# Optimization experiments

Hardware: AMD Instinct MI355X
Metric: run time of the kernel (lower is better)

Reference implementation:

```python
import math
import jax, jax.numpy as jnp
import numpy as np

B_, H_, L_, N_ = 64, 256, 1024, 64  # batch, n_feat, n_embd(=seq len), complex state modes (d_state=128 -> 64 conj pairs)


def setup_inputs() -> dict:
    key = jax.random.key(0)
    ks = jax.random.split(key, 12)
    x = jax.random.normal(ks[0], (B_, H_, L_), jnp.float32)
    t = jax.random.randint(ks[1], (B_,), 0, 1000)
    # AdaLayerNorm linear: n_embd -> 2*n_embd
    ada_w = jax.random.normal(ks[2], (2 * L_, L_), jnp.float32) * 0.02
    ada_b = jnp.zeros((2 * L_,), jnp.float32)
    # S4Layer prenorm (LayerNorm over n_feat, affine)
    norm_w = jnp.ones((H_,), jnp.float32)
    norm_b = jnp.zeros((H_,), jnp.float32)
    # S4D-style diagonal SSM parameters
    log_dt = math.log(0.001) + jax.random.uniform(ks[3], (H_,), jnp.float32) * (math.log(0.1) - math.log(0.001))
    A_re = jnp.full((H_, N_), math.log(0.5), jnp.float32)            # A_real = -exp(A_re) = -0.5
    A_im = jnp.ones((H_, 1), jnp.float32) * (math.pi * jnp.arange(N_, dtype=jnp.float32))[None, :]
    C_re = jax.random.normal(ks[4], (2, H_, N_), jnp.float32) * (N_ ** -0.5)  # 2 channels: bidirectional
    C_im = jax.random.normal(ks[5], (2, H_, N_), jnp.float32) * (N_ ** -0.5)
    D = jax.random.normal(ks[6], (H_,), jnp.float32)
    out_w = jax.random.normal(ks[7], (H_, H_), jnp.float32) * (H_ ** -0.5)   # S4 output 1x1 conv
    out_b = jnp.zeros((H_,), jnp.float32)
    lin1_w = jax.random.normal(ks[8], (H_, H_), jnp.float32) * (H_ ** -0.5)
    lin1_b = jnp.zeros((H_,), jnp.float32)
    lin2_w = jax.random.normal(ks[9], (H_, H_), jnp.float32) * (H_ ** -0.5)
    lin2_b = jnp.zeros((H_,), jnp.float32)
    return dict(x=x, t=t, ada_w=ada_w, ada_b=ada_b, norm_w=norm_w, norm_b=norm_b,
                log_dt=log_dt, A_re=A_re, A_im=A_im, C_re=C_re, C_im=C_im, D=D,
                out_w=out_w, out_b=out_b, lin1_w=lin1_w, lin1_b=lin1_b,
                lin2_w=lin2_w, lin2_b=lin2_b)


def _ln(v):
    m = v.mean(-1, keepdims=True)
    s = v.var(-1, keepdims=True)
    return (v - m) * jax.lax.rsqrt(s + 1e-5)


def _forward(t, x, ada_w, ada_b, norm_w, norm_b, log_dt, A_re, A_im, C_re, C_im, D,
             out_w, out_b, lin1_w, lin1_b, lin2_w, lin2_b):
    B, H, L = x.shape
    # ---- AdaLayerNorm over last dim (n_embd = L) ----
    half = L // 2
    freqs = jnp.exp(jnp.arange(half, dtype=jnp.float32) * (-math.log(10000.0) / (half - 1)))
    emb = t.astype(jnp.float32)[:, None] * freqs[None, :]
    emb = jnp.concatenate([jnp.sin(emb), jnp.cos(emb)], axis=-1)           # (B, L)
    emb = jax.nn.silu(emb) @ ada_w.T + ada_b                                # (B, 2L)
    scale, shift = jnp.split(emb[:, None, :], 2, axis=2)                    # (B,1,L)
    x = _ln(x) * (1.0 + scale) + shift                                      # (B,H,L)
    # ---- S4Layer: prenorm over channels ----
    z = (_ln(x.transpose(0, 2, 1)) * norm_w + norm_b).transpose(0, 2, 1)    # (B,H,L)
    # ---- S4 (diagonal SSM) bidirectional FFT convolution ----
    dt = jnp.exp(log_dt)                                                    # (H,)
    A = -jnp.exp(A_re) + 1j * A_im                                          # (H,N)
    dtA = dt[:, None] * A
    dA = jnp.exp(dtA)
    C = (C_re + 1j * C_im) * ((dA - 1.0) / A)                               # ZOH-discretized (2,H,N)
    vand = jnp.exp(dtA[:, :, None] * jnp.arange(L, dtype=jnp.float32))      # (H,N,L)
    K = 2.0 * jnp.real(jnp.einsum('chn,hnl->chl', C, vand))                 # (2,H,L)
    k = jnp.pad(K[0], ((0, 0), (0, L))) + jnp.pad(K[1][:, ::-1], ((0, 0), (L, 0)))  # (H,2L)
    n = 2 * L
    y = jnp.fft.irfft(jnp.fft.rfft(z, n=n) * jnp.fft.rfft(k, n=n), n=n)[..., :L]
    y = y + D[:, None] * z
    y = jax.nn.gelu(y, approximate=False)
    y = jnp.einsum('oi,bil->bol', out_w, y) + out_b[None, :, None]          # S4 output 1x1 conv
    x2 = y + x                                                              # residual
    # ---- gated output ----
    g = jnp.tanh(x2) * jax.nn.sigmoid(x2)
    out1 = jnp.einsum('oi,bil->bol', lin1_w, g) + lin1_b[None, :, None] + x
    out2 = jnp.einsum('oi,bil->bol', lin2_w, g) + lin2_b[None, :, None]
    return (out1, out2)


def reference(x, t, ada_w, ada_b, norm_w, norm_b, log_dt, A_re, A_im, C_re, C_im, D,
              out_w, out_b, lin1_w, lin1_b, lin2_w, lin2_b):
    return _forward(t, x, ada_w, ada_b, norm_w, norm_b, log_dt, A_re, A_im, C_re, C_im,
                    D, out_w, out_b, lin1_w, lin1_b, lin2_w, lin2_b)
```

## Files before the change

kernel.cpp:

```cpp
#include <hip/hip_runtime.h>
#include <math.h>

#define Bq 64
#define Hq 256
#define Lq 1024
#define HLq (Hq*Lq)
#define BHLq (Bq*Hq*Lq)
#define HNq (Hq*64)

typedef __attribute__((ext_vector_type(8))) short bf16x8;
typedef __attribute__((ext_vector_type(4))) float f32x4;

__device__ __forceinline__ float sigmoidf_(float x){ return 1.f/(1.f+expf(-x)); }
__device__ __forceinline__ unsigned short f2bf(float f){
  unsigned u = __float_as_uint(f);
  u += 0x7FFF + ((u>>16)&1);
  return (unsigned short)(u>>16);
}
__device__ __forceinline__ float bf2f(unsigned short h){ return __uint_as_float(((unsigned)h)<<16); }

__global__ __launch_bounds__(256) void k_ada2(const int* __restrict__ tptr,
        const float* __restrict__ ada_w, float* __restrict__ Part){
  __shared__ float Es[64][68];
  __shared__ float Ws[64][68];
  const int tid = threadIdx.x;
  const int o0 = blockIdx.x * 64;
  const int kc = blockIdx.y;
  const int k0 = kc * 64;
  const float ci = -logf(10000.f) / 511.f;
  #pragma unroll
  for (int it = 0; it < 4; ++it){
    int fidx = it*256 + tid;
    int row = fidx >> 4;
    int c4  = fidx & 15;
    float tb = (float)tptr[row];
    float4 v;
    float* vp = &v.x;
    #pragma unroll
    for (int q = 0; q < 4; ++q){
      int k = k0 + c4*4 + q;
      float f = expf(ci * (float)(k & 511));
      float arg = tb * f;
      float s = (k < 512) ? sinf(arg) : cosf(arg);
      vp[q] = s * sigmoidf_(s);
    }
    *(float4*)&Es[row][c4*4] = v;
  }
  #pragma unroll
  for (int it = 0; it < 4; ++it){
    int fidx = it*256 + tid;
    int row = fidx >> 4;
    int c4  = fidx & 15;
    *(float4*)&Ws[row][c4*4] = *(const float4*)(ada_w + (size_t)(o0+row)*1024 + k0 + c4*4);
  }
  __syncthreads();
  float acc[4][4] = {};
  #pragma unroll
  for (int ks = 0; ks < 16; ++ks){
    int k = ks*4;
    float4 ev[4], wv[4];
    #pragma unroll
    for (int i=0;i<4;++i) ev[i] = *(const float4*)&Es[(tid>>4) + 16*i][k];
    #pragma unroll
    for (int j=0;j<4;++j) wv[j] = *(const float4*)&Ws[(tid&15) + 16*j][k];
    #pragma unroll
    for (int i=0;i<4;++i)
      #pragma unroll
      for (int j=0;j<4;++j)
        acc[i][j] += ev[i].x*wv[j].x + ev[i].y*wv[j].y + ev[i].z*wv[j].z + ev[i].w*wv[j].w;
  }
  float* pbase = Part + (size_t)kc*131072 + o0;
  #pragma unroll
  for (int i=0;i<4;++i){
    int b = (tid>>4) + 16*i;
    #pragma unroll
    for (int j=0;j<4;++j){
      int o = (tid&15) + 16*j;
      pbase[(size_t)b*2048 + o] = acc[i][j];
    }
  }
}

__global__ void k_red(const float* __restrict__ Part, const float* __restrict__ ada_b,
                      float* __restrict__ scsh){
  int idx = blockIdx.x*256 + threadIdx.x;
  float4 s = ((const float4*)ada_b)[idx & 511];
  #pragma unroll
  for (int p = 0; p < 16; ++p){
    float4 u = ((const float4*)Part)[p*32768 + idx];
    s.x += u.x; s.y += u.y; s.z += u.z; s.w += u.w;
  }
  ((float4*)scsh)[idx] = s;
}

__global__ void k_wcvt(const float* __restrict__ w0, const float* __restrict__ w1,
                       const float* __restrict__ w2, unsigned short* __restrict__ wb){
  int idx = blockIdx.x*256 + threadIdx.x;
  const float* src = (idx < 16384) ? w0 : ((idx < 32768) ? w1 : w2);
  int loc = idx & 16383;
  float4 v = ((const float4*)src)[loc];
  uint2 pk;
  pk.x = (unsigned)f2bf(v.x) | ((unsigned)f2bf(v.y)<<16);
  pk.y = (unsigned)f2bf(v.z) | ((unsigned)f2bf(v.w)<<16);
  ((uint2*)wb)[idx] = pk;
}

__global__ void k_adaln(const float* __restrict__ x, const float* __restrict__ scsh,
                        float* __restrict__ A){
  const int bid = blockIdx.x;
  const int b = bid >> 8;
  const int tid = threadIdx.x;
  const float4* row = (const float4*)(x + (size_t)bid*1024);
  float4 v = row[tid];
  float s = v.x+v.y+v.z+v.w;
  float ss = v.x*v.x+v.y*v.y+v.z*v.z+v.w*v.w;
  #pragma unroll
  for (int off=32; off; off>>=1){ s += __shfl_xor(s,off); ss += __shfl_xor(ss,off); }
  __shared__ float rs_[4], rss_[4];
  int lane = tid & 63, w = tid >> 6;
  if (!lane){ rs_[w]=s; rss_[w]=ss; }
  __syncthreads();
  s  = rs_[0]+rs_[1]+rs_[2]+rs_[3];
  ss = rss_[0]+rss_[1]+rss_[2]+rss_[3];
  float mean = s * (1.f/1024.f);
  float var  = ss*(1.f/1024.f) - mean*mean;
  float rstd = rsqrtf(var + 1e-5f);
  float4 sc = ((const float4*)(scsh + b*2048))[tid];
  float4 sh = ((const float4*)(scsh + b*2048 + 1024))[tid];
  float4 o;
  o.x = (v.x-mean)*rstd*(1.f+sc.x) + sh.x;
  o.y = (v.y-mean)*rstd*(1.f+sc.y) + sh.y;
  o.z = (v.z-mean)*rstd*(1.f+sc.z) + sh.z;
  o.w = (v.w-mean)*rstd*(1.f+sc.w) + sh.w;
  ((float4*)(A + (size_t)bid*1024))[tid] = o;
}

__global__ void k_chln(const float* __restrict__ A, const float* __restrict__ nw,
                       const float* __restrict__ nb, unsigned short* __restrict__ Zb){
  const int b = blockIdx.y;
  const int l = blockIdx.x*256 + threadIdx.x;
  const float* base = A + (size_t)b*HLq + l;
  float s=0.f, ss=0.f;
  for (int h=0; h<256; ++h){ float v = base[h*1024]; s+=v; ss+=v*v; }
  float mean = s*(1.f/256.f);
  float var  = ss*(1.f/256.f) - mean*mean;
  float rstd = rsqrtf(var+1e-5f);
  unsigned short* zb = Zb + (size_t)b*HLq + l;
  for (int h=0; h<256; ++h){
    float v = base[h*1024];
    zb[h*1024] = f2bf((v-mean)*rstd*nw[h] + nb[h]);
  }
}

__global__ void k_ssmk(const float* __restrict__ log_dt, const float* __restrict__ A_re,
                       const float* __restrict__ A_im, const float* __restrict__ C_re,
                       const float* __restrict__ C_im, float* __restrict__ Kbuf){
  const int h = blockIdx.y;
  const int tid = threadIdx.x;
  __shared__ float dre[64], dim_[64], c0r[64], c0i[64], c1r[64], c1i[64];
  if (tid < 64){
    int n = tid;
    float dt = expf(log_dt[h]);
    float Ar = -expf(A_re[h*64+n]);
    float Ai = A_im[h*64+n];
    float dr = dt*Ar, di = dt*Ai;
    float er = expf(dr);
    float dAr = er*cosf(di), dAi = er*sinf(di);
    float den = Ar*Ar + Ai*Ai;
    float nr = dAr - 1.f, ni = dAi;
    float qr = (nr*Ar + ni*Ai)/den;
    float qi = (ni*Ar - nr*Ai)/den;
    float C0r = C_re[h*64+n],       C0i = C_im[h*64+n];
    float C1r = C_re[HNq + h*64+n], C1i = C_im[HNq + h*64+n];
    c0r[n] = C0r*qr - C0i*qi; c0i[n] = C0r*qi + C0i*qr;
    c1r[n] = C1r*qr - C1i*qi; c1i[n] = C1r*qi + C1i*qr;
    dre[n] = dr; dim_[n] = di;
  }
  __syncthreads();
  int l = blockIdx.x*256 + tid;
  float lf = (float)l;
  float a0=0.f, a1=0.f;
  for (int n=0;n<64;++n){
    float e  = expf(lf*dre[n]);
    float ph = lf*dim_[n];
    float wr = e*cosf(ph), wi = e*sinf(ph);
    a0 += c0r[n]*wr - c0i[n]*wi;
    a1 += c1r[n]*wr - c1i[n]*wi;
  }
  Kbuf[h*1024 + l]       = 2.f*a0;
  Kbuf[HLq + h*1024 + l] = 2.f*a1;
}

__global__ __launch_bounds__(256,2) void k_conv(const unsigned short* __restrict__ Zb,
        const float* __restrict__ Kbuf, const float* __restrict__ Dp,
        unsigned short* __restrict__ Cb){
  __shared__ unsigned short kcopy[8][2056];
  __shared__ unsigned short As[64][136];
  const int tid = threadIdx.x;
  const int h  = blockIdx.y;
  const int l0 = blockIdx.x * 512;
  const float* K0 = Kbuf + h*1024;
  const float* K1 = Kbuf + HLq + h*1024;
  for (int idx = tid; idx < 8*2056; idx += 256){
    int s = idx / 2056;
    int i = idx - s*2056;
    int q = 2046 - i - s;
    float v = 0.f;
    if (q >= 0) v = (q >= 1023) ? K0[q-1023] : K1[1022-q];
    kcopy[s][i] = f2bf(v);
  }
  const int lane = tid & 63;
  const int w    = tid >> 6;
  const int ln   = lane & 15;
  const int quad = lane >> 4;
  int kofs[8];
  #pragma unroll
  for (int nt=0; nt<8; ++nt){
    int l = l0 + w*128 + nt*16 + ln;
    int d = 1023 - l;
    int s = d & 7;
    kofs[nt] = s*2056 + (d - s) + quad*8;
  }
  const unsigned short* kbase = &kcopy[0][0];
  f32x4 acc[4][8] = {};
  for (int c = 0; c < 8; ++c){
    __syncthreads();
    #pragma unroll
    for (int pass = 0; pass < 4; ++pass){
      int b = pass*16 + (tid>>4);
      int col = (tid & 15)*8;
      *(uint4*)&As[b][col] = *(const uint4*)(Zb + ((size_t)b*256 + h)*1024 + c*128 + col);
    }
    __syncthreads();
    #pragma unroll
    for (int ks = 0; ks < 4; ++ks){
      int kk = ks*32 + quad*8;
      bf16x8 af[4];
      #pragma unroll
      for (int mt=0; mt<4; ++mt) af[mt] = *(const bf16x8*)&As[mt*16+ln][kk];
      int jb = c*128 + ks*32;
      bf16x8 bv[8];
      #pragma unroll
      for (int nt=0; nt<8; ++nt) bv[nt] = *(const bf16x8*)(kbase + kofs[nt] + jb);
      #pragma unroll
      for (int mt=0; mt<4; ++mt)
        #pragma unroll
        for (int nt=0; nt<8; ++nt)
          acc[mt][nt] = __builtin_amdgcn_mfma_f32_16x16x32_bf16(af[mt], bv[nt], acc[mt][nt], 0,0,0);
    }
  }
  float Dh = Dp[h];
  #pragma unroll
  for (int mt=0; mt<4; ++mt){
    #pragma unroll
    for (int reg=0; reg<4; ++reg){
      int b = mt*16 + quad*4 + reg;
      const unsigned short* zrow = Zb + ((size_t)b*256+h)*1024;
      unsigned short* crow = Cb + ((size_t)b*256+h)*1024;
      #pragma unroll
      for (int nt=0; nt<8; ++nt){
        int l = l0 + w*128 + nt*16 + ln;
        float y = acc[mt][nt][reg] + Dh*bf2f(zrow[l]);
        float g = 0.5f*y*(1.f + erff(y*0.70710678118f));
        crow[l] = f2bf(g);
      }
    }
  }
}

__global__ __launch_bounds__(256,2)
void k_fuse(const unsigned short* __restrict__ U,
        const unsigned short* __restrict__ Wob, const float* __restrict__ out_b,
        const unsigned short* __restrict__ W1b, const float* __restrict__ b1,
        const unsigned short* __restrict__ W2b, const float* __restrict__ b2,
        const float* __restrict__ Ax, float* __restrict__ out){
  __shared__ unsigned short Ts[32][264];
  const int tid = threadIdx.x;
  const int l0 = blockIdx.x * 32;
  const int b  = blockIdx.y;
  const int lane = tid & 63, w = tid >> 6, ln = lane & 15, quad = lane >> 4;
  {
    int l  = tid & 31;
    int g0 = tid >> 5;
    #pragma unroll
    for (int it = 0; it < 8; ++it){
      int i4 = it*8 + g0;
      const unsigned short* usrc = U + ((size_t)b*256 + i4*4)*1024 + l0 + l;
      unsigned short e0 = usrc[0], e1 = usrc[1024], e2 = usrc[2048], e3 = usrc[3072];
      uint2 val; val.x = (unsigned)e0 | ((unsigned)e1<<16); val.y = (unsigned)e2 | ((unsigned)e3<<16);
      *(uint2*)&Ts[l][i4*4] = val;
    }
  }
  __syncthreads();
  f32x4 acc1[4][2] = {};
  #pragma unroll
  for (int ks = 0; ks < 8; ++ks){
    int kk = ks*32 + quad*8;
    bf16x8 af[4], bv[2];
    #pragma unroll
    for (int mt=0;mt<4;++mt) af[mt] = *(const bf16x8*)(Wob + (size_t)(w*64+mt*16+ln)*256 + kk);
    #pragma unroll
    for (int nt=0;nt<2;++nt) bv[nt] = *(const bf16x8*)&Ts[nt*16+ln][kk];
    #pragma unroll
    for (int mt=0;mt<4;++mt)
      #pragma unroll
      for (int nt=0;nt<2;++nt)
        acc1[mt][nt] = __builtin_amdgcn_mfma_f32_16x16x32_bf16(af[mt], bv[nt], acc1[mt][nt],0,0,0);
  }
  #pragma unroll
  for (int mt=0;mt<4;++mt){
    #pragma unroll
    for (int reg=0;reg<4;++reg){
      int o = w*64 + mt*16 + quad*4 + reg;
      float bo = out_b[o];
      const float* arow = Ax + ((size_t)b*256 + o)*1024 + l0;
      #pragma unroll
      for (int nt=0;nt<2;++nt){
        int l = nt*16 + ln;
        float v = acc1[mt][nt][reg] + bo + arow[l];
        float t = expf(-fmaxf(v, -15.f));
        acc1[mt][nt][reg] = (1.f - t)/(1.f + t*t);
      }
    }
  }
  __syncthreads();
  #pragma unroll
  for (int mt=0;mt<4;++mt){
    int ob = w*64 + mt*16 + quad*4;
    #pragma unroll
    for (int nt=0;nt<2;++nt){
      int l = nt*16 + ln;
      uint2 pk;
      pk.x = (unsigned)f2bf(acc1[mt][nt][0]) | ((unsigned)f2bf(acc1[mt][nt][1])<<16);
      pk.y = (unsigned)f2bf(acc1[mt][nt][2]) | ((unsigned)f2bf(acc1[mt][nt][3])<<16);
      *(uint2*)&Ts[l][ob] = pk;
    }
  }
  __syncthreads();
  #pragma unroll
  for (int half = 0; half < 2; ++half){
    f32x4 accA[2][2] = {}, accB[2][2] = {};
    #pragma unroll
    for (int ks = 0; ks < 8; ++ks){
      int kk = ks*32 + quad*8;
      bf16x8 bv[2];
      #pragma unroll
      for (int nt=0;nt<2;++nt) bv[nt] = *(const bf16x8*)&Ts[nt*16+ln][kk];
      #pragma unroll
      for (int mt=0;mt<2;++mt){
        int orow = w*64 + (half*2+mt)*16 + ln;
        bf16x8 a1 = *(const bf16x8*)(W1b + (size_t)orow*256 + kk);
        #pragma unroll
        for (int nt=0;nt<2;++nt)
          accA[mt][nt] = __builtin_amdgcn_mfma_f32_16x16x32_bf16(a1, bv[nt], accA[mt][nt],0,0,0);
        bf16x8 a2 = *(const bf16x8*)(W2b + (size_t)orow*256 + kk);
        #pragma unroll
        for (int nt=0;nt<2;++nt)
          accB[mt][nt] = __builtin_amdgcn_mfma_f32_16x16x32_bf16(a2, bv[nt], accB[mt][nt],0,0,0);
      }
    }
    #pragma unroll
    for (int mt=0;mt<2;++mt){
      #pragma unroll
      for (int reg=0;reg<4;++reg){
        int o = w*64 + (half*2+mt)*16 + quad*4 + reg;
        float bo1 = b1[o], bo2 = b2[o];
        const float* arow = Ax + ((size_t)b*256 + o)*1024 + l0;
        float* o1row = out + ((size_t)b*256 + o)*1024 + l0;
        float* o2row = o1row + BHLq;
        #pragma unroll
        for (int nt=0;nt<2;++nt){
          int l = nt*16 + ln;
          o1row[l] = accA[mt][nt][reg] + bo1 + arow[l];
          o2row[l] = accB[mt][nt][reg] + bo2;
        }
      }
    }
  }
}

extern "C" void kernel_launch(void* const* d_in, const int* in_sizes, int n_in,
                              void* d_out, int out_size, void* d_ws, size_t ws_size,
                              hipStream_t stream){
  const float* x      = (const float*)d_in[0];
  const int*   t      = (const int*)  d_in[1];
  const float* ada_w  = (const float*)d_in[2];
  const float* ada_b  = (const float*)d_in[3];
  const float* norm_w = (const float*)d_in[4];
  const float* norm_b = (const float*)d_in[5];
  const float* log_dt = (const float*)d_in[6];
  const float* A_re   = (const float*)d_in[7];
  const float* A_im   = (const float*)d_in[8];
  const float* C_re   = (const float*)d_in[9];
  const float* C_im   = (const float*)d_in[10];
  const float* Dp     = (const float*)d_in[11];
  const float* out_w  = (const float*)d_in[12];
  const float* out_b  = (const float*)d_in[13];
  const float* lin1_w = (const float*)d_in[14];
  const float* lin1_b = (const float*)d_in[15];
  const float* lin2_w = (const float*)d_in[16];
  const float* lin2_b = (const float*)d_in[17];

  float* Ax            = (float*)d_ws;
  unsigned short* Zb   = (unsigned short*)(Ax + BHLq);
  unsigned short* Cb   = Zb + BHLq;
  float* Kbuf          = (float*)(Cb + BHLq);
  float* Part          = Kbuf + 2*HLq;
  float* scsh          = Part + 16*64*2048;
  unsigned short* wb   = (unsigned short*)(scsh + 64*2048);
  float* out           = (float*)d_out;

  k_wcvt  <<<192, 256, 0, stream>>>(out_w, lin1_w, lin2_w, wb);
  k_ada2  <<<dim3(32, 16), 256, 0, stream>>>(t, ada_w, Part);
  k_red   <<<128, 256, 0, stream>>>(Part, ada_b, scsh);
  k_adaln <<<Bq*Hq, 256, 0, stream>>>(x, scsh, Ax);
  k_chln  <<<dim3(4, Bq), 256, 0, stream>>>(Ax, norm_w, norm_b, Zb);
  k_ssmk  <<<dim3(4, Hq), 256, 0, stream>>>(log_dt, A_re, A_im, C_re, C_im, Kbuf);
  k_conv  <<<dim3(2, Hq), 256, 0, stream>>>(Zb, Kbuf, Dp, Cb);
  k_fuse  <<<dim3(32, Bq), 256, 0, stream>>>(Cb, wb, out_b, wb + 65536, lin1_b,
                                             wb + 131072, lin2_b, Ax, out);
}
```

Before: 504.5 us.

## Split channel LayerNorm into parallel stats pass and vectorized normalize pass

Replaces the single channel-LayerNorm kernel, which launched only 256 blocks with one thread looping over 256 channels twice, with two kernels. The first computes per-position sum and sum of squares using a 4-way channel split inside each block and a shared-memory reduction over 1024 blocks. The second is a fully parallel elementwise normalize that uses float4 loads and packed bf16 stores. This raises parallelism and vectorizes memory access, at the cost of an extra launch and a small stats round trip. The stats reuse the Part scratch buffer, which is no longer needed by that point.

Result: no change. 502.1 us (-0.5%).

```diff
diff --git a/kernel.cpp b/kernel.cpp
--- a/kernel.cpp
+++ b/kernel.cpp
@@ -135,21 +135,51 @@
   ((float4*)(A + (size_t)bid*1024))[tid] = o;
 }
 
-__global__ void k_chln(const float* __restrict__ A, const float* __restrict__ nw,
-                       const float* __restrict__ nb, unsigned short* __restrict__ Zb){
-  const int b = blockIdx.y;
-  const int l = blockIdx.x*256 + threadIdx.x;
-  const float* base = A + (size_t)b*HLq + l;
-  float s=0.f, ss=0.f;
-  for (int h=0; h<256; ++h){ float v = base[h*1024]; s+=v; ss+=v*v; }
-  float mean = s*(1.f/256.f);
-  float var  = ss*(1.f/256.f) - mean*mean;
-  float rstd = rsqrtf(var+1e-5f);
-  unsigned short* zb = Zb + (size_t)b*HLq + l;
-  for (int h=0; h<256; ++h){
-    float v = base[h*1024];
-    zb[h*1024] = f2bf((v-mean)*rstd*nw[h] + nb[h]);
-  }
+__global__ __launch_bounds__(256) void k_chst(const float* __restrict__ A,
+        float* __restrict__ S, float* __restrict__ SS){
+  const int b  = blockIdx.y;
+  const int lt = threadIdx.x & 63;
+  const int hc = threadIdx.x >> 6;
+  const int l  = blockIdx.x*64 + lt;
+  const float* p = A + (size_t)b*HLq + (size_t)hc*64*1024 + l;
+  float s = 0.f, ss = 0.f;
+  #pragma unroll 8
+  for (int h = 0; h < 64; ++h){ float v = p[(size_t)h*1024]; s += v; ss += v*v; }
+  __shared__ float sp[4][64], ssp[4][64];
+  sp[hc][lt] = s; ssp[hc][lt] = ss;
+  __syncthreads();
+  if (threadIdx.x < 64){
+    int li = threadIdx.x;
+    float st  = sp[0][li]+sp[1][li]+sp[2][li]+sp[3][li];
+    float sst = ssp[0][li]+ssp[1][li]+ssp[2][li]+ssp[3][li];
+    S [b*1024 + blockIdx.x*64 + li] = st;
+    SS[b*1024 + blockIdx.x*64 + li] = sst;
+  }
+}
+
+__global__ __launch_bounds__(256) void k_chnm(const float* __restrict__ A,
+        const float* __restrict__ S, const float* __restrict__ SS,
+        const float* __restrict__ nw, const float* __restrict__ nb,
+        unsigned short* __restrict__ Zb){
+  int idx = blockIdx.x*256 + threadIdx.x;
+  int b   = idx >> 16;
+  int rem = idx & 65535;
+  int h   = rem >> 8;
+  int l4  = rem & 255;
+  float4 v  = ((const float4*)(A + (size_t)b*HLq + (size_t)h*1024))[l4];
+  float4 s4 = ((const float4*)(S  + b*1024))[l4];
+  float4 q4 = ((const float4*)(SS + b*1024))[l4];
+  float w_ = nw[h], bb = nb[h];
+  float m, r;
+  unsigned short ox, oy, oz, ow;
+  m = s4.x*(1.f/256.f); r = rsqrtf(q4.x*(1.f/256.f) - m*m + 1e-5f); ox = f2bf((v.x-m)*r*w_ + bb);
+  m = s4.y*(1.f/256.f); r = rsqrtf(q4.y*(1.f/256.f) - m*m + 1e-5f); oy = f2bf((v.y-m)*r*w_ + bb);
+  m = s4.z*(1.f/256.f); r = rsqrtf(q4.z*(1.f/256.f) - m*m + 1e-5f); oz = f2bf((v.z-m)*r*w_ + bb);
+  m = s4.w*(1.f/256.f); r = rsqrtf(q4.w*(1.f/256.f) - m*m + 1e-5f); ow = f2bf((v.w-m)*r*w_ + bb);
+  uint2 pk;
+  pk.x = (unsigned)ox | ((unsigned)oy<<16);
+  pk.y = (unsigned)oz | ((unsigned)ow<<16);
+  ((uint2*)Zb)[idx] = pk;
 }
 
 __global__ void k_ssmk(const float* __restrict__ log_dt, const float* __restrict__ A_re,
@@ -408,13 +438,16 @@
   float* Part          = Kbuf + 2*HLq;
   float* scsh          = Part + 16*64*2048;
   unsigned short* wb   = (unsigned short*)(scsh + 64*2048);
+  float* Sst           = Part;
+  float* SSst          = Part + 65536;
   float* out           = (float*)d_out;
 
   k_wcvt  <<<192, 256, 0, stream>>>(out_w, lin1_w, lin2_w, wb);
   k_ada2  <<<dim3(32, 16), 256, 0, stream>>>(t, ada_w, Part);
   k_red   <<<128, 256, 0, stream>>>(Part, ada_b, scsh);
   k_adaln <<<Bq*Hq, 256, 0, stream>>>(x, scsh, Ax);
-  k_chln  <<<dim3(4, Bq), 256, 0, stream>>>(Ax, norm_w, norm_b, Zb);
+  k_chst  <<<dim3(16, Bq), 256, 0, stream>>>(Ax, Sst, SSst);
+  k_chnm  <<<16384, 256, 0, stream>>>(Ax, Sst, SSst, norm_w, norm_b, Zb);
   k_ssmk  <<<dim3(4, Hq), 256, 0, stream>>>(log_dt, A_re, A_im, C_re, C_im, Kbuf);
   k_conv  <<<dim3(2, Hq), 256, 0, stream>>>(Zb, Kbuf, Dp, Cb);
   k_fuse  <<<dim3(32, Bq), 256, 0, stream>>>(Cb, wb, out_b, wb + 65536, lin1_b,
```
